# Kernel tuning notes

Measured on AMD Instinct MI355X. Metric: run time of the kernel, lower is better.

## Reference

```python
import jax, jax.numpy as jnp
import numpy as np

RC = 4.6  # cutoff radius (Angstrom), from init_kwargs
FACTOR = 7.199822675975224  # constants.half_Hartree * constants.Bohr (eV*A)


def exp_cutoff(d, rc):
    # smooth exponential (bump) cutoff: exp(1 - 1/(1-(d/rc)^2)) for d<rc, else 0
    x = d / rc
    inside = x < 1.0
    xs = jnp.where(inside, x, 0.5)  # safe value to avoid nan in masked branch
    f = jnp.exp(1.0 - 1.0 / (1.0 - xs * xs))
    return jnp.where(inside, f, 0.0)


def setup_inputs() -> dict:
    key = jax.random.key(0)
    k1, k2 = jax.random.split(key)
    B, N = 64, 512
    # atoms in a 40 A box -> realistic long-range distances
    coord = jax.random.uniform(k1, (B, N, 3), dtype=jnp.float32) * 40.0
    charges = jax.random.normal(k2, (B, N), dtype=jnp.float32) * 0.3
    mask = jnp.ones((B, N), dtype=bool)  # all atoms valid (no padding)
    return {"coord": coord, "charges": charges, "mask": mask}


def reference(coord, charges, mask):
    # coul_simple: e = factor * sum_ij (1 - fc(d_ij)) * q_i * q_j / d_ij, per molecule
    B, N, _ = coord.shape
    pair_mask = mask[:, :, None] & mask[:, None, :]
    eye = jnp.eye(N, dtype=bool)[None]
    valid = pair_mask & ~eye  # mask self-pairs and padding (mask_ij_)
    disp = coord[:, :, None, :] - coord[:, None, :, :]          # [B,N,N,3]
    d2 = jnp.sum(disp * disp, axis=-1)                          # [B,N,N]
    d = jnp.sqrt(jnp.where(valid, d2, 1.0))                     # safe sqrt on diag
    fc = 1.0 - exp_cutoff(d, RC)
    qq = charges[:, :, None] * charges[:, None, :]              # q_i * q_j
    e_ij = jnp.where(valid, fc * qq / d, 0.0)
    return FACTOR * jnp.sum(e_ij, axis=(1, 2))                  # mol_sum -> [B]
```

## Files before the change

kernel.cpp:

```cpp
#include <hip/hip_runtime.h>

#define N_ATOMS 512
#define BLOCK   1024
#define FACTOR  7.199822675975224f
#define RC2     (4.6f * 4.6f)

__global__ __launch_bounds__(BLOCK) void coul_mol_kernel(
    const float* __restrict__ coord,
    const float* __restrict__ charges,
    float* __restrict__ out)
{
    const int b = blockIdx.x;
    const int t = threadIdx.x;

    __shared__ float4 atom[2 * N_ATOMS];

    const float* c = coord   + (size_t)b * N_ATOMS * 3;
    const float* q = charges + (size_t)b * N_ATOMS;
    if (t < N_ATOMS) {
        float4 a = make_float4(c[3 * t], c[3 * t + 1], c[3 * t + 2], q[t]);
        atom[t]           = a;
        atom[t + N_ATOMS] = a;
    }
    __syncthreads();

    const int i = t & (N_ATOMS - 1);
    const int h = t >> 9;
    const float4 ai = atom[i];
    const float inv_rc2 = 1.0f / RC2;
    const float4* __restrict__ base = &atom[i + 1 + h * 128];

    float acc = 0.0f;
    #pragma unroll 8
    for (int k = 0; k < 127; ++k) {
        const float4 aj = base[k];
        float dx = ai.x - aj.x, dy = ai.y - aj.y, dz = ai.z - aj.z;
        float d2 = dx * dx + dy * dy + dz * dz;
        float term = aj.w * rsqrtf(d2);
        if (d2 < RC2)
            term *= (1.0f - __expf(1.0f - 1.0f / (1.0f - d2 * inv_rc2)));
        acc += term;
    }
    {
        const float4 aj = base[127];
        float dx = ai.x - aj.x, dy = ai.y - aj.y, dz = ai.z - aj.z;
        float d2 = dx * dx + dy * dy + dz * dz;
        float term = aj.w * rsqrtf(d2);
        if (d2 < RC2)
            term *= (1.0f - __expf(1.0f - 1.0f / (1.0f - d2 * inv_rc2)));
        acc += h ? 0.5f * term : term;
    }
    acc *= ai.w;

    #pragma unroll
    for (int off = 32; off > 0; off >>= 1)
        acc += __shfl_down(acc, off, 64);

    __shared__ float wsum[BLOCK / 64];
    if ((t & 63) == 0) wsum[t >> 6] = acc;
    __syncthreads();
    if (t == 0) {
        float sum = 0.0f;
        #pragma unroll
        for (int w = 0; w < BLOCK / 64; ++w) sum += wsum[w];
        out[b] = 2.0f * FACTOR * sum;
    }
}

extern "C" void kernel_launch(void* const* d_in, const int* in_sizes, int n_in,
                              void* d_out, int out_size, void* d_ws, size_t ws_size,
                              hipStream_t stream) {
    const float* coord   = (const float*)d_in[0];
    const float* charges = (const float*)d_in[1];
    float* out = (float*)d_out;
    (void)d_ws; (void)ws_size;

    const int B = (n_in > 2 && in_sizes[1] != in_sizes[2])
                      ? in_sizes[1] / (N_ATOMS * 4)
                      : in_sizes[1] / N_ATOMS;

    coul_mol_kernel<<<B, BLOCK, 0, stream>>>(coord, charges, out);
}
```

Before: 77.41 us.

## Split each molecule across eight blocks and reduce partials in a second kernel

Each molecule's pair sum is split into eight j-chunks, each handled by a 512-thread block, so the grid grows from one block per molecule to eight. The symmetric half-pair trick is dropped, so every i,j pair is computed and the self-pair is masked. Partial sums go to workspace and a small second kernel adds them. This spreads work over many more compute units at the cost of doubled arithmetic and an extra launch.

```diff
diff --git a/kernel.cpp b/kernel.cpp
--- a/kernel.cpp
+++ b/kernel.cpp
@@ -1,54 +1,43 @@
 #include <hip/hip_runtime.h>
 
 #define N_ATOMS 512
-#define BLOCK   1024
+#define JSPLIT  8
+#define JLEN    (N_ATOMS / JSPLIT)
+#define BLOCK   512
 #define FACTOR  7.199822675975224f
 #define RC2     (4.6f * 4.6f)
 
-__global__ __launch_bounds__(BLOCK) void coul_mol_kernel(
+__global__ __launch_bounds__(BLOCK) void coul_pair_kernel(
     const float* __restrict__ coord,
     const float* __restrict__ charges,
-    float* __restrict__ out)
+    float* __restrict__ partials)
 {
-    const int b = blockIdx.x;
-    const int t = threadIdx.x;
+    const int b = blockIdx.x >> 3;
+    const int s = blockIdx.x & 7;
 
-    __shared__ float4 atom[2 * N_ATOMS];
+    __shared__ float4 atom[N_ATOMS];
 
     const float* c = coord   + (size_t)b * N_ATOMS * 3;
     const float* q = charges + (size_t)b * N_ATOMS;
-    if (t < N_ATOMS) {
-        float4 a = make_float4(c[3 * t], c[3 * t + 1], c[3 * t + 2], q[t]);
-        atom[t]           = a;
-        atom[t + N_ATOMS] = a;
-    }
+    const int t = threadIdx.x;
+    atom[t] = make_float4(c[3 * t], c[3 * t + 1], c[3 * t + 2], q[t]);
     __syncthreads();
 
-    const int i = t & (N_ATOMS - 1);
-    const int h = t >> 9;
+    const int i = t;
     const float4 ai = atom[i];
     const float inv_rc2 = 1.0f / RC2;
-    const float4* __restrict__ base = &atom[i + 1 + h * 128];
+    const float4* __restrict__ base = &atom[s * JLEN];
 
     float acc = 0.0f;
     #pragma unroll 8
-    for (int k = 0; k < 127; ++k) {
+    for (int k = 0; k < JLEN; ++k) {
         const float4 aj = base[k];
         float dx = ai.x - aj.x, dy = ai.y - aj.y, dz = ai.z - aj.z;
         float d2 = dx * dx + dy * dy + dz * dz;
         float term = aj.w * rsqrtf(d2);
         if (d2 < RC2)
             term *= (1.0f - __expf(1.0f - 1.0f / (1.0f - d2 * inv_rc2)));
-        acc += term;
-    }
-    {
-        const float4 aj = base[127];
-        float dx = ai.x - aj.x, dy = ai.y - aj.y, dz = ai.z - aj.z;
-        float d2 = dx * dx + dy * dy + dz * dz;
-        float term = aj.w * rsqrtf(d2);
-        if (d2 < RC2)
-            term *= (1.0f - __expf(1.0f - 1.0f / (1.0f - d2 * inv_rc2)));
-        acc += h ? 0.5f * term : term;
+        acc += (s * JLEN + k == i) ? 0.0f : term;
     }
     acc *= ai.w;
 
@@ -63,7 +52,19 @@
         float sum = 0.0f;
         #pragma unroll
         for (int w = 0; w < BLOCK / 64; ++w) sum += wsum[w];
-        out[b] = 2.0f * FACTOR * sum;
+        partials[blockIdx.x] = sum;
+    }
+}
+
+__global__ void coul_reduce_kernel(const float* __restrict__ partials,
+                                   float* __restrict__ out, int B)
+{
+    const int b = threadIdx.x;
+    if (b < B) {
+        float sum = 0.0f;
+        #pragma unroll
+        for (int s = 0; s < JSPLIT; ++s) sum += partials[b * JSPLIT + s];
+        out[b] = FACTOR * sum;
     }
 }
 
@@ -72,12 +73,13 @@
                               hipStream_t stream) {
     const float* coord   = (const float*)d_in[0];
     const float* charges = (const float*)d_in[1];
-    float* out = (float*)d_out;
-    (void)d_ws; (void)ws_size;
+    float* out      = (float*)d_out;
+    float* partials = (float*)d_ws;
 
     const int B = (n_in > 2 && in_sizes[1] != in_sizes[2])
                       ? in_sizes[1] / (N_ATOMS * 4)
                       : in_sizes[1] / N_ATOMS;
 
-    coul_mol_kernel<<<B, BLOCK, 0, stream>>>(coord, charges, out);
+    coul_pair_kernel<<<B * JSPLIT, BLOCK, 0, stream>>>(coord, charges, partials);
+    coul_reduce_kernel<<<1, 64, 0, stream>>>(partials, out, B);
 }
```

Result: faster. 73.42 us (-5.2%).
